# Performance work log

Measured on AMD Instinct MI355X. Metric: run time of the kernel, lower is better.

## Reference

```python
import jax, jax.numpy as jnp
import numpy as np

EPS = 1e-5

@jax.custom_vjp
def sign_ste(x):
    # binarize to {-1, +1}; sign(0) maps to +1 as in most binary-net impls
    return jnp.where(x >= 0, 1.0, -1.0).astype(x.dtype)

def _sign_fwd(x):
    return sign_ste(x), x

def _sign_bwd(x, g):
    # straight-through estimator with hardtanh clipping
    return (g * (jnp.abs(x) <= 1.0).astype(g.dtype),)

sign_ste.defvjp(_sign_fwd, _sign_bwd)


def setup_inputs() -> dict:
    key = jax.random.key(0)
    k1, k2, k3 = jax.random.split(key, 3)
    N, Cin, Cout = 65536, 1024, 1024
    return {
        "x": jax.random.normal(k1, (N, Cin), dtype=jnp.float32),
        "gamma": jnp.ones((Cin,), dtype=jnp.float32),
        "beta": jnp.zeros((Cin,), dtype=jnp.float32),
        "W": jax.random.normal(k2, (Cout, Cin), dtype=jnp.float32) * 0.03,
        "b": jnp.zeros((Cout,), dtype=jnp.float32),
        "scale": jnp.ones((Cout,), dtype=jnp.float32),
        "alpha": jnp.float32(0.25),
    }


def reference(x, gamma, beta, W, b, scale, alpha):
    # 1) BatchNorm1d centering (training-mode batch statistics over nodes)
    mu = jnp.mean(x, axis=0)
    var = jnp.var(x, axis=0)
    xh = (x - mu) * jax.lax.rsqrt(var + EPS) * gamma + beta
    # 2) STE binarize activations
    xq = sign_ste(xh)
    # 3) binary linear: sign(W) GEMM + bias  -> [N, Cout]
    wq = sign_ste(W)
    y = jnp.einsum('nc,oc->no', xq, wq) + b
    # 4) learned per-channel rescale
    y = y * scale
    # 5) PReLU
    return jnp.where(y > 0, y, alpha * y)
```

## Files before the change

kernel.cpp:

```cpp
#include <hip/hip_runtime.h>
#include <stdint.h>
#include <math.h>

#define NROWS 65536
#define CIN   1024
#define COUT  1024
#define BN_EPS 1e-5

static constexpr size_t OFF_PSUM = 0;
static constexpr size_t OFF_PSQ  = 8ull  * 1024 * 1024;
static constexpr size_t OFF_MU   = 16ull * 1024 * 1024;
static constexpr size_t OFF_INV  = 16ull * 1024 * 1024 + 4096;
static constexpr size_t OFF_W8   = 17ull * 1024 * 1024;
static constexpr size_t OFF_A8   = 24ull * 1024 * 1024;

typedef int i32x4 __attribute__((ext_vector_type(4)));

__device__ __forceinline__ void gload_lds16(const void* g, void* l) {
  __builtin_amdgcn_global_load_lds(
      (const __attribute__((address_space(1))) uint32_t*)g,
      (__attribute__((address_space(3))) uint32_t*)l, 16, 0, 0);
}

__global__ __launch_bounds__(256) void k_stats_partial(
    const float* __restrict__ x, double* __restrict__ psum, double* __restrict__ psq) {
  int tid = threadIdx.x;
  size_t r0 = (size_t)blockIdx.x * 64;
  const float4* xp = (const float4*)x + r0 * 256 + tid;
  double s0 = 0, s1 = 0, s2 = 0, s3 = 0;
  double q0 = 0, q1 = 0, q2 = 0, q3 = 0;
  for (int r = 0; r < 64; r += 8) {
    float4 v[8];
#pragma unroll
    for (int u = 0; u < 8; ++u) v[u] = xp[(size_t)(r + u) * 256];
#pragma unroll
    for (int u = 0; u < 8; ++u) {
      double a = (double)v[u].x, b = (double)v[u].y;
      double c = (double)v[u].z, d = (double)v[u].w;
      s0 += a; q0 = fma(a, a, q0);
      s1 += b; q1 = fma(b, b, q1);
      s2 += c; q2 = fma(c, c, q2);
      s3 += d; q3 = fma(d, d, q3);
    }
  }
  size_t base = (size_t)blockIdx.x * CIN + (size_t)tid * 4;
  double2* ps = (double2*)(psum + base);
  ps[0] = make_double2(s0, s1);
  ps[1] = make_double2(s2, s3);
  double2* pq = (double2*)(psq + base);
  pq[0] = make_double2(q0, q1);
  pq[1] = make_double2(q2, q3);
}

__global__ __launch_bounds__(256) void k_stats_final(
    const double* __restrict__ psum, const double* __restrict__ psq,
    float* __restrict__ mu, float* __restrict__ inv) {
  __shared__ double sd[16][16];
  __shared__ double sq[16][16];
  int tid = threadIdx.x;
  int cl = tid & 15;
  int g  = tid >> 4;
  int col = blockIdx.x * 16 + cl;
  double s = 0, q = 0;
  for (int i = 0; i < 64; ++i) {
    size_t chunk = (size_t)(g * 64 + i);
    s += psum[chunk * CIN + col];
    q += psq [chunk * CIN + col];
  }
  sd[g][cl] = s;
  sq[g][cl] = q;
  __syncthreads();
  if (tid < 16) {
    s = 0; q = 0;
#pragma unroll
    for (int i = 0; i < 16; ++i) { s += sd[i][tid]; q += sq[i][tid]; }
    double mean = s / (double)NROWS;
    double var  = q / (double)NROWS - mean * mean;
    int c = blockIdx.x * 16 + tid;
    mu[c]  = (float)mean;
    inv[c] = (float)(1.0 / sqrt(var + (double)BN_EPS));
  }
}

__global__ __launch_bounds__(256) void k_binarize_x(
    const float* __restrict__ x, const float* __restrict__ mu,
    const float* __restrict__ inv, const float* __restrict__ gamma,
    const float* __restrict__ beta, uint32_t* __restrict__ A8) {
  int tid = threadIdx.x;
  float4 M  = ((const float4*)mu)[tid];
  float4 I  = ((const float4*)inv)[tid];
  float4 G  = ((const float4*)gamma)[tid];
  float4 Bt = ((const float4*)beta)[tid];
  size_t n0 = (size_t)blockIdx.x * 8;
  const float4* xp = (const float4*)x + n0 * 256 + tid;
  for (int r = 0; r < 8; ++r) {
    float4 v = xp[(size_t)r * 256];
    float h0 = ((v.x - M.x) * I.x) * G.x + Bt.x;
    float h1 = ((v.y - M.y) * I.y) * G.y + Bt.y;
    float h2 = ((v.z - M.z) * I.z) * G.z + Bt.z;
    float h3 = ((v.w - M.w) * I.w) * G.w + Bt.w;
    uint32_t p = (h0 >= 0.0f ? 0x01u : 0xFFu)
               | ((h1 >= 0.0f ? 0x01u : 0xFFu) << 8)
               | ((h2 >= 0.0f ? 0x01u : 0xFFu) << 16)
               | ((h3 >= 0.0f ? 0x01u : 0xFFu) << 24);
    A8[(n0 + r) * 256 + tid] = p;
  }
}

__global__ __launch_bounds__(256) void k_binarize_w(
    const float* __restrict__ W, uint32_t* __restrict__ W8) {
  int tid = threadIdx.x;
  size_t o0 = (size_t)blockIdx.x * 8;
  const float4* wp = (const float4*)W + o0 * 256 + tid;
  for (int r = 0; r < 8; ++r) {
    float4 v = wp[(size_t)r * 256];
    uint32_t p = (v.x >= 0.0f ? 0x01u : 0xFFu)
               | ((v.y >= 0.0f ? 0x01u : 0xFFu) << 8)
               | ((v.z >= 0.0f ? 0x01u : 0xFFu) << 16)
               | ((v.w >= 0.0f ? 0x01u : 0xFFu) << 24);
    W8[(o0 + r) * 256 + tid] = p;
  }
}

__global__ __launch_bounds__(512, 4) void k_mmi8(
    const int8_t* __restrict__ A8, const int8_t* __restrict__ W8,
    const float* __restrict__ bias, const float* __restrict__ scale,
    const float* __restrict__ alphaPtr, float* __restrict__ out) {
  __shared__ uint8_t As[128 * 128];
  __shared__ uint8_t Bs[256 * 128];
  int tid  = threadIdx.x;
  int lane = tid & 63, wv = tid >> 6;
  int wr = wv >> 2, wc = wv & 3;
  size_t n0 = (size_t)blockIdx.y * 128;
  int c0 = blockIdx.x * 256;

  i32x4 acc[4][4] = {};

  int rsub = tid >> 3;
  int swzc = ((tid & 7) ^ (rsub & 7)) << 4;
  const int8_t* Asrc = A8 + (n0 + (size_t)rsub) * 1024 + swzc;
  const int8_t* Bsrc = W8 + ((size_t)c0 + rsub) * 1024 + swzc;

  for (int t = 0; t < 8; ++t) {
#pragma unroll
    for (int i = 0; i < 2; ++i)
      gload_lds16(Asrc + (size_t)i * 64 * 1024 + t * 128, &As[i * 8192 + wv * 1024]);
#pragma unroll
    for (int i = 0; i < 4; ++i)
      gload_lds16(Bsrc + (size_t)i * 64 * 1024 + t * 128, &Bs[i * 8192 + wv * 1024]);
    __syncthreads();

#pragma unroll
    for (int kk = 0; kk < 2; ++kk) {
      int colb = (kk * 64 + ((lane >> 4) << 4)) ^ ((lane & 7) << 4);
      i32x4 af[4], bf[4];
#pragma unroll
      for (int m = 0; m < 4; ++m) {
        int row = wr * 64 + m * 16 + (lane & 15);
        af[m] = *(const i32x4*)&As[row * 128 + colb];
      }
#pragma unroll
      for (int n = 0; n < 4; ++n) {
        int row = wc * 64 + n * 16 + (lane & 15);
        bf[n] = *(const i32x4*)&Bs[row * 128 + colb];
      }
#pragma unroll
      for (int m = 0; m < 4; ++m)
#pragma unroll
        for (int n = 0; n < 4; ++n)
          acc[m][n] = __builtin_amdgcn_mfma_i32_16x16x64_i8(af[m], bf[n], acc[m][n], 0, 0, 0);
    }
    __syncthreads();
  }

  float alpha = alphaPtr[0];
#pragma unroll
  for (int n = 0; n < 4; ++n) {
    int col = c0 + wc * 64 + n * 16 + (lane & 15);
    float b  = bias[col];
    float sc = scale[col];
#pragma unroll
    for (int m = 0; m < 4; ++m) {
      size_t rbase = n0 + (size_t)wr * 64 + m * 16 + ((lane >> 4) << 2);
#pragma unroll
      for (int r = 0; r < 4; ++r) {
        float y = ((float)acc[m][n][r] + b) * sc;
        out[(rbase + r) * COUT + col] = y > 0.0f ? y : alpha * y;
      }
    }
  }
}

extern "C" void kernel_launch(void* const* d_in, const int* in_sizes, int n_in,
                              void* d_out, int out_size, void* d_ws, size_t ws_size,
                              hipStream_t stream) {
  const float* x     = (const float*)d_in[0];
  const float* gamma = (const float*)d_in[1];
  const float* beta  = (const float*)d_in[2];
  const float* W     = (const float*)d_in[3];
  const float* b     = (const float*)d_in[4];
  const float* scale = (const float*)d_in[5];
  const float* alpha = (const float*)d_in[6];
  float* out = (float*)d_out;

  char* ws = (char*)d_ws;
  double*   psum = (double*)(ws + OFF_PSUM);
  double*   psq  = (double*)(ws + OFF_PSQ);
  float*    mu   = (float*)(ws + OFF_MU);
  float*    inv  = (float*)(ws + OFF_INV);
  uint32_t* W8   = (uint32_t*)(ws + OFF_W8);
  uint32_t* A8   = (uint32_t*)(ws + OFF_A8);

  k_stats_partial<<<dim3(NROWS / 64), 256, 0, stream>>>(x, psum, psq);
  k_stats_final<<<dim3(CIN / 16), 256, 0, stream>>>(psum, psq, mu, inv);
  k_binarize_w<<<dim3(COUT / 8), 256, 0, stream>>>(W, W8);
  k_binarize_x<<<dim3(NROWS / 8), 256, 0, stream>>>(x, mu, inv, gamma, beta, A8);
  k_mmi8<<<dim3(COUT / 256, NROWS / 128), 512, 0, stream>>>(
      (const int8_t*)A8, (const int8_t*)W8, b, scale, alpha, out);
}
```

Measured before the change: 600.8 us.

## Merge binarize kernels, reverse x order, remap GEMM blocks across XCDs

Merges the W and x binarization kernels into one launch. The x blocks now walk the rows in reverse, so the rows of x that k_stats_partial read last (and that may still sit in L2/MALL) are touched first. The GEMM block index is remapped so that consecutive blocks on each XCD share row tiles of A, which should improve L2 reuse. The epilogue stores are also reordered so each thread writes all four n-columns of one row together. Together these aim to cut launch overhead and DRAM traffic, at the cost of more complex block mapping.

```diff
diff --git a/kernel.cpp b/kernel.cpp
--- a/kernel.cpp
+++ b/kernel.cpp
@@ -82,16 +82,30 @@
   }
 }
 
-__global__ __launch_bounds__(256) void k_binarize_x(
+__global__ __launch_bounds__(256) void k_binarize(
     const float* __restrict__ x, const float* __restrict__ mu,
     const float* __restrict__ inv, const float* __restrict__ gamma,
-    const float* __restrict__ beta, uint32_t* __restrict__ A8) {
+    const float* __restrict__ beta, const float* __restrict__ W,
+    uint32_t* __restrict__ A8, uint32_t* __restrict__ W8) {
   int tid = threadIdx.x;
+  if (blockIdx.x >= 8192) {
+    size_t o0 = (size_t)(blockIdx.x - 8192) * 8;
+    const float4* wp = (const float4*)W + o0 * 256 + tid;
+    for (int r = 0; r < 8; ++r) {
+      float4 v = wp[(size_t)r * 256];
+      uint32_t p = (v.x >= 0.0f ? 0x01u : 0xFFu)
+                 | ((v.y >= 0.0f ? 0x01u : 0xFFu) << 8)
+                 | ((v.z >= 0.0f ? 0x01u : 0xFFu) << 16)
+                 | ((v.w >= 0.0f ? 0x01u : 0xFFu) << 24);
+      W8[(o0 + r) * 256 + tid] = p;
+    }
+    return;
+  }
   float4 M  = ((const float4*)mu)[tid];
   float4 I  = ((const float4*)inv)[tid];
   float4 G  = ((const float4*)gamma)[tid];
   float4 Bt = ((const float4*)beta)[tid];
-  size_t n0 = (size_t)blockIdx.x * 8;
+  size_t n0 = (size_t)(8191 - blockIdx.x) * 8;
   const float4* xp = (const float4*)x + n0 * 256 + tid;
   for (int r = 0; r < 8; ++r) {
     float4 v = xp[(size_t)r * 256];
@@ -107,21 +121,6 @@
   }
 }
 
-__global__ __launch_bounds__(256) void k_binarize_w(
-    const float* __restrict__ W, uint32_t* __restrict__ W8) {
-  int tid = threadIdx.x;
-  size_t o0 = (size_t)blockIdx.x * 8;
-  const float4* wp = (const float4*)W + o0 * 256 + tid;
-  for (int r = 0; r < 8; ++r) {
-    float4 v = wp[(size_t)r * 256];
-    uint32_t p = (v.x >= 0.0f ? 0x01u : 0xFFu)
-               | ((v.y >= 0.0f ? 0x01u : 0xFFu) << 8)
-               | ((v.z >= 0.0f ? 0x01u : 0xFFu) << 16)
-               | ((v.w >= 0.0f ? 0x01u : 0xFFu) << 24);
-    W8[(o0 + r) * 256 + tid] = p;
-  }
-}
-
 __global__ __launch_bounds__(512, 4) void k_mmi8(
     const int8_t* __restrict__ A8, const int8_t* __restrict__ W8,
     const float* __restrict__ bias, const float* __restrict__ scale,
@@ -131,8 +130,13 @@
   int tid  = threadIdx.x;
   int lane = tid & 63, wv = tid >> 6;
   int wr = wv >> 2, wc = wv & 3;
-  size_t n0 = (size_t)blockIdx.y * 128;
-  int c0 = blockIdx.x * 256;
+
+  int lin = blockIdx.x + (int)blockIdx.y * 4;
+  int nl  = (lin & 7) * 256 + (lin >> 3);
+  int bx  = nl & 3;
+  int by  = nl >> 2;
+  size_t n0 = (size_t)by * 128;
+  int c0 = bx * 256;
 
   i32x4 acc[4][4] = {};
 
@@ -174,18 +178,23 @@
   }
 
   float alpha = alphaPtr[0];
+  float bz[4], sc4[4];
 #pragma unroll
   for (int n = 0; n < 4; ++n) {
     int col = c0 + wc * 64 + n * 16 + (lane & 15);
-    float b  = bias[col];
-    float sc = scale[col];
-#pragma unroll
-    for (int m = 0; m < 4; ++m) {
-      size_t rbase = n0 + (size_t)wr * 64 + m * 16 + ((lane >> 4) << 2);
-#pragma unroll
-      for (int r = 0; r < 4; ++r) {
-        float y = ((float)acc[m][n][r] + b) * sc;
-        out[(rbase + r) * COUT + col] = y > 0.0f ? y : alpha * y;
+    bz[n]  = bias[col];
+    sc4[n] = scale[col];
+  }
+#pragma unroll
+  for (int m = 0; m < 4; ++m) {
+    size_t rbase = n0 + (size_t)wr * 64 + m * 16 + ((lane >> 4) << 2);
+#pragma unroll
+    for (int r = 0; r < 4; ++r) {
+      float* orow = out + (rbase + r) * COUT + c0 + wc * 64 + (lane & 15);
+#pragma unroll
+      for (int n = 0; n < 4; ++n) {
+        float y = ((float)acc[m][n][r] + bz[n]) * sc4[n];
+        orow[n * 16] = y > 0.0f ? y : alpha * y;
       }
     }
   }
@@ -213,8 +222,8 @@
 
   k_stats_partial<<<dim3(NROWS / 64), 256, 0, stream>>>(x, psum, psq);
   k_stats_final<<<dim3(CIN / 16), 256, 0, stream>>>(psum, psq, mu, inv);
-  k_binarize_w<<<dim3(COUT / 8), 256, 0, stream>>>(W, W8);
-  k_binarize_x<<<dim3(NROWS / 8), 256, 0, stream>>>(x, mu, inv, gamma, beta, A8);
+  k_binarize<<<dim3(NROWS / 8 + COUT / 8), 256, 0, stream>>>(
+      x, mu, inv, gamma, beta, W, A8, W8);
   k_mmi8<<<dim3(COUT / 256, NROWS / 128), 512, 0, stream>>>(
       (const int8_t*)A8, (const int8_t*)W8, b, scale, alpha, out);
 }
```

Measured after the change: 593.1 us. No clear change (-1.3%).
